# Performance work log

Hardware: AMD Instinct MI355X
Metric: run time of the kernel (lower is better)

The kernel has to match this reference:

```python
import jax, jax.numpy as jnp
import numpy as np

V, E, H = 32000, 512, 1024  # vocab, embed_dim, hidden_dim
N, T = 32, 256              # batch, seq_len


def setup_inputs() -> dict:
    key = jax.random.key(0)
    ks = jax.random.split(key, 8)
    s = 1.0 / np.sqrt(H)
    return {
        "words": jax.random.randint(ks[0], (N, T), 0, V),
        "hidden_state": jnp.zeros((N, H), jnp.float32),
        "embed_w": jax.random.uniform(ks[1], (V, E), minval=-1.0, maxval=1.0) * 0.1,
        "w_ih": jax.random.uniform(ks[2], (3 * H, E), minval=-s, maxval=s),
        "w_hh": jax.random.uniform(ks[3], (3 * H, H), minval=-s, maxval=s),
        "b_ih": jax.random.uniform(ks[4], (3 * H,), minval=-s, maxval=s),
        "b_hh": jax.random.uniform(ks[5], (3 * H,), minval=-s, maxval=s),
        "emit_w": jax.random.uniform(ks[6], (V, H), minval=-s, maxval=s),
        "emit_b": jnp.zeros((V,), jnp.float32),
    }


def reference(words, hidden_state, embed_w, w_ih, w_hh, b_ih, b_hh, emit_w, emit_b):
    n = words.shape[0]
    emb = embed_w[words]                      # [N, T, E]
    xs = (jnp.swapaxes(emb[:, :-1], 0, 1),    # [T-1, N, E] inputs x_{t-1}
          jnp.swapaxes(words[:, 1:], 0, 1))   # [T-1, N]    targets w_t

    def gru_cell(x, h):
        gi = x @ w_ih.T + b_ih                # [N, 3H]
        gh = h @ w_hh.T + b_hh                # [N, 3H]
        i_r, i_z, i_n = jnp.split(gi, 3, axis=-1)
        h_r, h_z, h_n = jnp.split(gh, 3, axis=-1)
        r = jax.nn.sigmoid(i_r + h_r)
        z = jax.nn.sigmoid(i_z + h_z)
        nn_ = jnp.tanh(i_n + r * h_n)
        return (1.0 - z) * nn_ + z * h

    def step(carry, inp):
        h, acc = carry
        x, w = inp
        h = gru_cell(x, h)
        logits = h @ emit_w.T + emit_b        # [N, V]
        logp = jax.nn.log_softmax(logits, axis=-1)
        ll = jnp.take_along_axis(logp, w[:, None], axis=1)[:, 0]  # [N]
        return (h, acc + ll), None

    acc0 = jnp.zeros((n,), hidden_state.dtype)
    (h_final, word_marginals), _ = jax.lax.scan(step, (hidden_state, acc0), xs)
    return word_marginals, h_final
```

## Files before the change

kernel.cpp:

```cpp
#include <hip/hip_runtime.h>
#include <cstdint>

#define V_    32000
#define E_    512
#define H_    1024
#define N_    32
#define T_    256
#define TS    255
#define NWG_B 64
#define CB_   250
#define RB_   64
#define MROW  8192
#define GI_CB 24

typedef _Float16 f16;
typedef _Float16 half8 __attribute__((ext_vector_type(8)));
typedef float floatx4 __attribute__((ext_vector_type(4)));
typedef unsigned long long u64;


__global__ void prep_emit16(const float* __restrict__ emit_w, f16* __restrict__ out) {
  const int64_t nchunk = (int64_t)V_ * H_ / 8;
  int64_t i = (int64_t)blockIdx.x * blockDim.x + threadIdx.x;
  for (; i < nchunk; i += (int64_t)gridDim.x * blockDim.x) {
    const float4* src = (const float4*)(emit_w + i * 8);
    float4 a = src[0], b = src[1];
    half8 h;
    h[0] = (f16)a.x; h[1] = (f16)a.y; h[2] = (f16)a.z; h[3] = (f16)a.w;
    h[4] = (f16)b.x; h[5] = (f16)b.y; h[6] = (f16)b.z; h[7] = (f16)b.w;
    *(half8*)(out + i * 8) = h;
  }
}

__global__ void prep_whh(const float* __restrict__ w_hh, f16* __restrict__ whh) {
  int idx = blockIdx.x * blockDim.x + threadIdx.x;
  if (idx >= 192 * 32 * 64) return;
  int lane = idx & 63;
  int kt   = (idx >> 6) & 31;
  int jt   = (idx >> 6) >> 5;
  int col  = jt * 16 + (lane & 15);
  int k0   = kt * 32 + (lane >> 4) * 8;
  const float* src = w_hh + (int64_t)col * H_ + k0;
  half8 h;
#pragma unroll
  for (int i = 0; i < 8; ++i) h[i] = (f16)src[i];
  *(half8*)(whh + (int64_t)idx * 8) = h;
}

__global__ void prep_wih16(const float* __restrict__ w_ih, f16* __restrict__ out) {
  int idx = blockIdx.x * blockDim.x + threadIdx.x;
  if (idx >= 3072 * 512 / 8) return;
  const float4* src = (const float4*)(w_ih + (int64_t)idx * 8);
  float4 a = src[0], b = src[1];
  half8 h;
  h[0] = (f16)a.x; h[1] = (f16)a.y; h[2] = (f16)a.z; h[3] = (f16)a.w;
  h[4] = (f16)b.x; h[5] = (f16)b.y; h[6] = (f16)b.z; h[7] = (f16)b.w;
  *(half8*)(out + (int64_t)idx * 8) = h;
}

__global__ void prep_xemb(const int* __restrict__ words, const float* __restrict__ embed_w,
                          f16* __restrict__ xemb) {
  int idx = blockIdx.x * blockDim.x + threadIdx.x;
  if (idx >= TS * N_ * (E_ / 8)) return;
  int u = idx & 63;
  int n = (idx >> 6) & 31;
  int t = idx >> 11;
  int word = words[n * T_ + t];
  const float* src = embed_w + (int64_t)word * E_ + u * 8;
  half8 h;
#pragma unroll
  for (int i = 0; i < 8; ++i) h[i] = (f16)src[i];
  *(half8*)(xemb + (int64_t)(t * N_ + n) * E_ + u * 8) = h;
}

__global__ void prep_init(const float* __restrict__ h0, f16* __restrict__ xh,
                          unsigned* __restrict__ slots) {
  int idx = blockIdx.x * blockDim.x + threadIdx.x;
  if (idx < N_ * H_) {
    f16 v = (f16)h0[idx];
    xh[idx] = v;
    xh[N_ * H_ + idx] = v;
  }
  if (idx < 1024) slots[idx] = 0;
}


#define LDK 72

__launch_bounds__(256, 2)
__global__ void gi_gemm(const f16* __restrict__ xemb, const f16* __restrict__ wih16,
                        f16* __restrict__ gi2) {
  const int cb = blockIdx.x % GI_CB;
  const int rb = blockIdx.x / GI_CB;
  const int tid = threadIdx.x;
  const int w = tid >> 6, lane = tid & 63;
  const int wm = w & 1, wn = w >> 1;
  const int l15 = lane & 15, l4 = lane >> 4;

  __shared__ f16 lA[128 * LDK];
  __shared__ f16 lB[128 * LDK];

  floatx4 acc[4][4];
#pragma unroll
  for (int mt = 0; mt < 4; ++mt)
#pragma unroll
    for (int nt = 0; nt < 4; ++nt) { acc[mt][nt][0] = 0.f; acc[mt][nt][1] = 0.f; acc[mt][nt][2] = 0.f; acc[mt][nt][3] = 0.f; }

  const f16* gA = xemb + (int64_t)rb * 128 * E_;
  const f16* gB = wih16 + (int64_t)cb * 128 * E_;

  for (int kb = 0; kb < 8; ++kb) {
    __syncthreads();
#pragma unroll
    for (int i = 0; i < 4; ++i) {
      int idx = i * 256 + tid;
      int row = idx >> 3, u = idx & 7;
      int64_t goff = (int64_t)row * E_ + kb * 64 + u * 8;
      *(half8*)(lA + row * LDK + u * 8) = *(const half8*)(gA + goff);
      *(half8*)(lB + row * LDK + u * 8) = *(const half8*)(gB + goff);
    }
    __syncthreads();
#pragma unroll
    for (int ks = 0; ks < 2; ++ks) {
      half8 af[4], bf[4];
#pragma unroll
      for (int mt = 0; mt < 4; ++mt)
        af[mt] = *(const half8*)(lA + (wm * 64 + mt * 16 + l15) * LDK + ks * 32 + l4 * 8);
#pragma unroll
      for (int nt = 0; nt < 4; ++nt)
        bf[nt] = *(const half8*)(lB + (wn * 64 + nt * 16 + l15) * LDK + ks * 32 + l4 * 8);
#pragma unroll
      for (int mt = 0; mt < 4; ++mt)
#pragma unroll
        for (int nt = 0; nt < 4; ++nt)
          acc[mt][nt] = __builtin_amdgcn_mfma_f32_16x16x32_f16(af[mt], bf[nt], acc[mt][nt], 0, 0, 0);
    }
  }

#pragma unroll
  for (int mt = 0; mt < 4; ++mt) {
#pragma unroll
    for (int r = 0; r < 4; ++r) {
      int g = rb * 128 + wm * 64 + mt * 16 + l4 * 4 + r;
      if (g < TS * N_) {
        int tt = g >> 5, n = g & 31;
        f16* gb = gi2 + ((int64_t)tt * 3072 + cb * 128 + wn * 64) * 32 + n;
#pragma unroll
        for (int nt = 0; nt < 4; ++nt)
          gb[(nt * 16 + l15) * 32] = (f16)acc[mt][nt][r];
      }
    }
  }
}


__device__ inline u64 aload64(const void* p) {
  return __hip_atomic_load((const u64*)p, __ATOMIC_RELAXED, __HIP_MEMORY_SCOPE_AGENT);
}
__device__ inline unsigned aload32(const void* p) {
  return __hip_atomic_load((const unsigned*)p, __ATOMIC_RELAXED, __HIP_MEMORY_SCOPE_AGENT);
}

__device__ inline void gbar3(unsigned* slots, unsigned tval, int b) {
  __syncthreads();
  if (threadIdx.x == 0) {
    __builtin_amdgcn_s_waitcnt(0);
    __hip_atomic_store(slots + b * 16, tval, __ATOMIC_RELAXED, __HIP_MEMORY_SCOPE_AGENT);
  }
  if (threadIdx.x < 64) {
    unsigned* my = slots + threadIdx.x * 16;
    while (__hip_atomic_load(my, __ATOMIC_RELAXED, __HIP_MEMORY_SCOPE_AGENT) < tval)
      __builtin_amdgcn_s_sleep(1);
  }
  __syncthreads();
}

__launch_bounds__(512, 1)
__global__ void phaseB(const f16* __restrict__ whh, const f16* __restrict__ gi2,
                       f16* __restrict__ xh, const float* __restrict__ b_ih,
                       const float* __restrict__ b_hh, f16* __restrict__ hall,
                       float* __restrict__ out, unsigned* __restrict__ slots) {
  const int b = blockIdx.x;
  const int tid = threadIdx.x;
  const int w = tid >> 6;
  const int lane = tid & 63;
  const int l15 = lane & 15, l4 = lane >> 4;

  __shared__ float part[8][32][49];

  const int n_g = tid & 31;
  const int jl = tid >> 5;
  const int j = b * 16 + jl;
  const float biasr = b_ih[j] + b_hh[j];
  const float biasz = b_ih[H_ + j] + b_hh[H_ + j];
  const float bihn = b_ih[2 * H_ + j];
  const float bhhn = b_hh[2 * H_ + j];

  half8 wf[3][4];
#pragma unroll
  for (int g = 0; g < 3; ++g) {
    int jt = g * 64 + b;
#pragma unroll
    for (int k = 0; k < 4; ++k)
      wf[g][k] = *(const half8*)(whh + (((int64_t)jt * 32 + (w * 4 + k)) * 64 + lane) * 8);
  }

  for (int t = 0; t < TS; ++t) {
    const f16* xh_rd = xh + (t & 1) * (N_ * H_);
    f16* xh_wr = xh + ((t + 1) & 1) * (N_ * H_);

    const f16* gbase = gi2 + (int64_t)t * 3072 * 32 + n_g;
    float gvr = (float)gbase[(int64_t)j * 32];
    float gvz = (float)gbase[(int64_t)(H_ + j) * 32];
    float gvn = (float)gbase[(int64_t)(2 * H_ + j) * 32];
    unsigned hraw = aload32(xh_rd + n_g * H_ + (j & ~1));
    unsigned short hbits = (jl & 1) ? (unsigned short)(hraw >> 16) : (unsigned short)(hraw & 0xffffu);
    float hold = (float)__builtin_bit_cast(f16, hbits);

    floatx4 acc[3][2];
#pragma unroll
    for (int g = 0; g < 3; ++g)
#pragma unroll
      for (int m = 0; m < 2; ++m) { acc[g][m][0] = 0.f; acc[g][m][1] = 0.f; acc[g][m][2] = 0.f; acc[g][m][3] = 0.f; }

    half8 a0[4], a1[4];
#pragma unroll
    for (int k = 0; k < 4; ++k) {
      const f16* base = xh_rd + (w * 4 + k) * 32 + l4 * 8;
      union { half8 h; u64 u[2]; } x0, x1;
      const u64* p0 = (const u64*)(base + (int64_t)l15 * H_);
      const u64* p1 = (const u64*)(base + (int64_t)(l15 + 16) * H_);
      x0.u[0] = aload64(p0); x0.u[1] = aload64(p0 + 1);
      x1.u[0] = aload64(p1); x1.u[1] = aload64(p1 + 1);
      a0[k] = x0.h; a1[k] = x1.h;
    }
#pragma unroll
    for (int k = 0; k < 4; ++k) {
#pragma unroll
      for (int g = 0; g < 3; ++g) {
        acc[g][0] = __builtin_amdgcn_mfma_f32_16x16x32_f16(a0[k], wf[g][k], acc[g][0], 0, 0, 0);
        acc[g][1] = __builtin_amdgcn_mfma_f32_16x16x32_f16(a1[k], wf[g][k], acc[g][1], 0, 0, 0);
      }
    }

#pragma unroll
    for (int g = 0; g < 3; ++g)
#pragma unroll
      for (int m = 0; m < 2; ++m)
#pragma unroll
        for (int r = 0; r < 4; ++r)
          part[w][m * 16 + l4 * 4 + r][g * 16 + l15] = acc[g][m][r];
    __syncthreads();

    float gr = biasr + gvr, gz = biasz + gvz, gin = bihn + gvn, ghn = bhhn;
#pragma unroll
    for (int ww = 0; ww < 8; ++ww) {
      gr += part[ww][n_g][jl];
      gz += part[ww][n_g][16 + jl];
      ghn += part[ww][n_g][32 + jl];
    }
    float rg = 1.f / (1.f + __expf(-gr));
    float zg = 1.f / (1.f + __expf(-gz));
    float nn = tanhf(gin + rg * ghn);
    float hnew = (1.f - zg) * nn + zg * hold;

    unsigned short hb = __builtin_bit_cast(unsigned short, (f16)hnew);
    unsigned other = (unsigned)__shfl_xor((int)(unsigned)hb, 32, 64);
    if (!(jl & 1)) {
      unsigned packed = (unsigned)hb | (other << 16);
      __hip_atomic_store((unsigned*)(xh_wr + n_g * H_ + j), packed,
                         __ATOMIC_RELAXED, __HIP_MEMORY_SCOPE_AGENT);
      *(unsigned*)(hall + ((int64_t)t * N_ + n_g) * H_ + j) = packed;
    }
    if (t == TS - 1) out[32 + n_g * H_ + j] = hnew;

    if (t < TS - 1) gbar3(slots, (unsigned)(t + 1), b);
  }
}


__launch_bounds__(256, 2)
__global__ void phaseC(const f16* __restrict__ hall, const f16* __restrict__ emit16,
                       const float* __restrict__ emit_b, float* __restrict__ spart) {
  const int cb = blockIdx.x % CB_;
  const int rb = blockIdx.x / CB_;
  const int tid = threadIdx.x;
  const int w = tid >> 6, lane = tid & 63;
  const int wm = w & 1, wn = w >> 1;
  const int l15 = lane & 15, l4 = lane >> 4;

  __shared__ f16 lA[128 * LDK];
  __shared__ f16 lB[128 * LDK];
  __shared__ float rs[2][128];

  floatx4 acc[4][4];
#pragma unroll
  for (int mt = 0; mt < 4; ++mt)
#pragma unroll
    for (int nt = 0; nt < 4; ++nt) { acc[mt][nt][0] = 0.f; acc[mt][nt][1] = 0.f; acc[mt][nt][2] = 0.f; acc[mt][nt][3] = 0.f; }

  const f16* gA = hall + (int64_t)rb * 128 * H_;
  const f16* gB = emit16 + (int64_t)cb * 128 * H_;

  for (int kb = 0; kb < 16; ++kb) {
    __syncthreads();
#pragma unroll
    for (int i = 0; i < 4; ++i) {
      int idx = i * 256 + tid;
      int row = idx >> 3, u = idx & 7;
      int64_t goff = (int64_t)row * H_ + kb * 64 + u * 8;
      *(half8*)(lA + row * LDK + u * 8) = *(const half8*)(gA + goff);
      *(half8*)(lB + row * LDK + u * 8) = *(const half8*)(gB + goff);
    }
    __syncthreads();
#pragma unroll
    for (int ks = 0; ks < 2; ++ks) {
      half8 af[4], bf[4];
#pragma unroll
      for (int mt = 0; mt < 4; ++mt)
        af[mt] = *(const half8*)(lA + (wm * 64 + mt * 16 + l15) * LDK + ks * 32 + l4 * 8);
#pragma unroll
      for (int nt = 0; nt < 4; ++nt)
        bf[nt] = *(const half8*)(lB + (wn * 64 + nt * 16 + l15) * LDK + ks * 32 + l4 * 8);
#pragma unroll
      for (int mt = 0; mt < 4; ++mt)
#pragma unroll
        for (int nt = 0; nt < 4; ++nt)
          acc[mt][nt] = __builtin_amdgcn_mfma_f32_16x16x32_f16(af[mt], bf[nt], acc[mt][nt], 0, 0, 0);
    }
  }

  float eb[4];
#pragma unroll
  for (int nt = 0; nt < 4; ++nt) eb[nt] = emit_b[cb * 128 + wn * 64 + nt * 16 + l15];

#pragma unroll
  for (int mt = 0; mt < 4; ++mt) {
#pragma unroll
    for (int r = 0; r < 4; ++r) {
      float s = 0.f;
#pragma unroll
      for (int nt = 0; nt < 4; ++nt) s += __expf(acc[mt][nt][r] + eb[nt]);
#pragma unroll
      for (int off = 1; off < 16; off <<= 1) s += __shfl_xor(s, off, 64);
      if (l15 == 0) rs[wn][wm * 64 + mt * 16 + l4 * 4 + r] = s;
    }
  }
  __syncthreads();
  if (tid < 128)
    spart[(int64_t)cb * MROW + rb * 128 + tid] = rs[0][tid] + rs[1][tid];
}


__global__ void target_dots(const f16* __restrict__ hall, const f16* __restrict__ emit16,
                            const int* __restrict__ words, const float* __restrict__ emit_b,
                            float* __restrict__ tlog) {
  int r = blockIdx.x * 4 + (threadIdx.x >> 6);
  if (r >= TS * N_) return;
  int lane = threadIdx.x & 63;
  int t = r >> 5, n = r & 31;
  int tgt = words[n * T_ + t + 1];
  const f16* ha = hall + (int64_t)r * H_;
  const f16* ebp = emit16 + (int64_t)tgt * H_;
  float s = 0.f;
#pragma unroll
  for (int c = 0; c < 2; ++c) {
    int k = c * 512 + lane * 8;
    half8 a = *(const half8*)(ha + k);
    half8 b = *(const half8*)(ebp + k);
#pragma unroll
    for (int i = 0; i < 8; ++i) s += (float)a[i] * (float)b[i];
  }
#pragma unroll
  for (int off = 1; off < 64; off <<= 1) s += __shfl_xor(s, off, 64);
  if (lane == 0) tlog[r] = s + emit_b[tgt];
}

__global__ void reduce_lse(const float* __restrict__ spart, const float* __restrict__ tlog,
                           float* __restrict__ lval) {
  int r = blockIdx.x * blockDim.x + threadIdx.x;
  if (r >= TS * N_) return;
  float s = 0.f;
  for (int cb = 0; cb < CB_; ++cb) s += spart[(int64_t)cb * MROW + r];
  lval[r] = tlog[r] - logf(s);
}

__global__ void finalize(const float* __restrict__ lval, float* __restrict__ out) {
  __shared__ float ps[8][32];
  int n = threadIdx.x & 31, sl = threadIdx.x >> 5;
  float s = 0.f;
  for (int i = 0; i < 32; ++i) {
    int t = sl * 32 + i;
    if (t < TS) s += lval[t * N_ + n];
  }
  ps[sl][n] = s;
  __syncthreads();
  if (threadIdx.x < 32) {
    float tot = 0.f;
#pragma unroll
    for (int k = 0; k < 8; ++k) tot += ps[k][threadIdx.x];
    out[threadIdx.x] = tot;
  }
}


extern "C" void kernel_launch(void* const* d_in, const int* in_sizes, int n_in,
                              void* d_out, int out_size, void* d_ws, size_t ws_size,
                              hipStream_t stream) {
  (void)in_sizes; (void)n_in; (void)out_size; (void)ws_size;
  const int*   words   = (const int*)d_in[0];
  const float* h0      = (const float*)d_in[1];
  const float* embed_w = (const float*)d_in[2];
  const float* w_ih    = (const float*)d_in[3];
  const float* w_hh    = (const float*)d_in[4];
  const float* b_ih    = (const float*)d_in[5];
  const float* b_hh    = (const float*)d_in[6];
  const float* emit_w  = (const float*)d_in[7];
  const float* emit_b  = (const float*)d_in[8];
  float* out = (float*)d_out;

  char* ws = (char*)d_ws;
  f16*      big    = (f16*)(ws + 0);
  f16*      gi2    = big;
  f16*      emit16 = big;
  f16*      whh    = (f16*)(ws + 65536000);
  f16*      wih16  = (f16*)(ws + 71827456);
  float*    spart  = (float*)(ws + 71827456);
  f16*      xemb   = (f16*)(ws + 74973184);
  f16*      xh     = (f16*)(ws + 83361792);
  f16*      hall   = (f16*)(ws + 83492864);
  float*    tlog   = (float*)(ws + 100270080);
  float*    lval   = (float*)(ws + 100302720);
  unsigned* slots  = (unsigned*)(ws + 100335360);

  hipLaunchKernelGGL(prep_whh, dim3(1536), dim3(256), 0, stream, w_hh, whh);
  hipLaunchKernelGGL(prep_wih16, dim3(768), dim3(256), 0, stream, w_ih, wih16);
  hipLaunchKernelGGL(prep_xemb, dim3(2040), dim3(256), 0, stream, words, embed_w, xemb);
  hipLaunchKernelGGL(prep_init, dim3(128), dim3(256), 0, stream, h0, xh, slots);
  hipLaunchKernelGGL(gi_gemm, dim3(RB_ * GI_CB), dim3(256), 0, stream, xemb, wih16, gi2);
  hipLaunchKernelGGL(phaseB, dim3(NWG_B), dim3(512), 0, stream, whh, gi2, xh, b_ih, b_hh, hall, out, slots);
  hipLaunchKernelGGL(prep_emit16, dim3(4096), dim3(256), 0, stream, emit_w, emit16);
  hipLaunchKernelGGL(phaseC, dim3(RB_ * CB_), dim3(256), 0, stream, hall, emit16, emit_b, spart);
  hipLaunchKernelGGL(target_dots, dim3((TS * N_ + 3) / 4), dim3(256), 0, stream, hall, emit16, words, emit_b, tlog);
  hipLaunchKernelGGL(reduce_lse, dim3((TS * N_ + 255) / 256), dim3(256), 0, stream, spart, tlog, lval);
  hipLaunchKernelGGL(finalize, dim3(1), dim3(256), 0, stream, lval, out);
}
```

Measured before the change: 2.728 ms.

## Replace grid barrier with per-element step-tagged hidden state flags

Drops the per-timestep global barrier in the persistent GRU recurrence kernel. Each fp16 hidden value is now stored next to a 16-bit step tag inside 64-bit words. Consumers spin until all the words they read carry the expected tag, so each block waits only on the data it needs instead of on every block. This removes the barrier's atomic round trips but doubles the size of the hidden-state exchange buffer and adds polling and unpacking work. It also reuses the xemb workspace region for the tagged buffer, which is safe only because the launch order was changed so gi_gemm runs first.

After: 4.452 ms. 1.63x slower.

```diff
diff --git a/kernel.cpp b/kernel.cpp
--- a/kernel.cpp
+++ b/kernel.cpp
@@ -73,15 +73,16 @@
   *(half8*)(xemb + (int64_t)(t * N_ + n) * E_ + u * 8) = h;
 }
 
-__global__ void prep_init(const float* __restrict__ h0, f16* __restrict__ xh,
-                          unsigned* __restrict__ slots) {
+__global__ void prep_init(const float* __restrict__ h0, u64* __restrict__ xt) {
   int idx = blockIdx.x * blockDim.x + threadIdx.x;
-  if (idx < N_ * H_) {
-    f16 v = (f16)h0[idx];
-    xh[idx] = v;
-    xh[N_ * H_ + idx] = v;
-  }
-  if (idx < 1024) slots[idx] = 0;
+  if (idx < N_ * H_ / 2) {
+    int n = idx >> 9;
+    int p = idx & 511;
+    unsigned short e = __builtin_bit_cast(unsigned short, (f16)h0[n * H_ + 2 * p]);
+    unsigned short o = __builtin_bit_cast(unsigned short, (f16)h0[n * H_ + 2 * p + 1]);
+    xt[idx] = (u64)(unsigned)e | ((u64)(unsigned)o << 32);
+    xt[N_ * H_ / 2 + idx] = 0;
+  }
 }
 
 
@@ -157,36 +158,19 @@
 __device__ inline u64 aload64(const void* p) {
   return __hip_atomic_load((const u64*)p, __ATOMIC_RELAXED, __HIP_MEMORY_SCOPE_AGENT);
 }
-__device__ inline unsigned aload32(const void* p) {
-  return __hip_atomic_load((const unsigned*)p, __ATOMIC_RELAXED, __HIP_MEMORY_SCOPE_AGENT);
-}
-
-__device__ inline void gbar3(unsigned* slots, unsigned tval, int b) {
-  __syncthreads();
-  if (threadIdx.x == 0) {
-    __builtin_amdgcn_s_waitcnt(0);
-    __hip_atomic_store(slots + b * 16, tval, __ATOMIC_RELAXED, __HIP_MEMORY_SCOPE_AGENT);
-  }
-  if (threadIdx.x < 64) {
-    unsigned* my = slots + threadIdx.x * 16;
-    while (__hip_atomic_load(my, __ATOMIC_RELAXED, __HIP_MEMORY_SCOPE_AGENT) < tval)
-      __builtin_amdgcn_s_sleep(1);
-  }
-  __syncthreads();
-}
 
 __launch_bounds__(512, 1)
 __global__ void phaseB(const f16* __restrict__ whh, const f16* __restrict__ gi2,
-                       f16* __restrict__ xh, const float* __restrict__ b_ih,
+                       u64* __restrict__ xt, const float* __restrict__ b_ih,
                        const float* __restrict__ b_hh, f16* __restrict__ hall,
-                       float* __restrict__ out, unsigned* __restrict__ slots) {
+                       float* __restrict__ out) {
   const int b = blockIdx.x;
   const int tid = threadIdx.x;
   const int w = tid >> 6;
   const int lane = tid & 63;
   const int l15 = lane & 15, l4 = lane >> 4;
 
-  __shared__ float part[8][32][49];
+  __shared__ float part[2][8][32][49];
 
   const int n_g = tid & 31;
   const int jl = tid >> 5;
@@ -205,17 +189,72 @@
       wf[g][k] = *(const half8*)(whh + (((int64_t)jt * 32 + (w * 4 + k)) * 64 + lane) * 8);
   }
 
+  {
+  }
+  u64 w0 = xt[n_g * (H_ / 2) + (j >> 1)];
+  unsigned lohi0 = (jl & 1) ? (unsigned)(w0 >> 32) : (unsigned)w0;
+  float hold = (float)__builtin_bit_cast(f16, (unsigned short)(lohi0 & 0xffffu));
+
   for (int t = 0; t < TS; ++t) {
-    const f16* xh_rd = xh + (t & 1) * (N_ * H_);
-    f16* xh_wr = xh + ((t + 1) & 1) * (N_ * H_);
+    const u64* xr = xt + (t & 1) * (N_ * (H_ / 2));
+    u64* xw = xt + ((t + 1) & 1) * (N_ * (H_ / 2));
+    const unsigned tg = (unsigned)t;
 
     const f16* gbase = gi2 + (int64_t)t * 3072 * 32 + n_g;
     float gvr = (float)gbase[(int64_t)j * 32];
     float gvz = (float)gbase[(int64_t)(H_ + j) * 32];
     float gvn = (float)gbase[(int64_t)(2 * H_ + j) * 32];
-    unsigned hraw = aload32(xh_rd + n_g * H_ + (j & ~1));
-    unsigned short hbits = (jl & 1) ? (unsigned short)(hraw >> 16) : (unsigned short)(hraw & 0xffffu);
-    float hold = (float)__builtin_bit_cast(f16, hbits);
+
+    half8 a0[4], a1[4];
+    {
+      u64 v[4][2][4];
+      bool ok[4][2] = {{false, false}, {false, false}, {false, false}, {false, false}};
+      int nleft = 8;
+      const u64* rp0 = xr + (int64_t)l15 * (H_ / 2) + l4 * 4;
+      const u64* rp1 = xr + (int64_t)(l15 + 16) * (H_ / 2) + l4 * 4;
+      while (true) {
+#pragma unroll
+        for (int k = 0; k < 4; ++k) {
+          if (!ok[k][0]) {
+            const u64* p = rp0 + (w * 4 + k) * 16;
+#pragma unroll
+            for (int q = 0; q < 4; ++q) v[k][0][q] = aload64(p + q);
+          }
+          if (!ok[k][1]) {
+            const u64* p = rp1 + (w * 4 + k) * 16;
+#pragma unroll
+            for (int q = 0; q < 4; ++q) v[k][1][q] = aload64(p + q);
+          }
+        }
+#pragma unroll
+        for (int k = 0; k < 4; ++k)
+#pragma unroll
+          for (int r = 0; r < 2; ++r) {
+            if (!ok[k][r]) {
+              bool f = true;
+#pragma unroll
+              for (int q = 0; q < 4; ++q) {
+                u64 x = v[k][r][q];
+                f = f && (((unsigned)(x >> 16) & 0xffffu) == tg) && ((unsigned)(x >> 48) == tg);
+              }
+              if (f) { ok[k][r] = true; --nleft; }
+            }
+          }
+        if (nleft == 0) break;
+        __builtin_amdgcn_s_sleep(1);
+      }
+#pragma unroll
+      for (int k = 0; k < 4; ++k) {
+        union { half8 h; unsigned u[4]; } t0, t1;
+#pragma unroll
+        for (int q = 0; q < 4; ++q) {
+          u64 x0 = v[k][0][q], x1 = v[k][1][q];
+          t0.u[q] = ((unsigned)x0 & 0xffffu) | (((unsigned)(x0 >> 32)) << 16);
+          t1.u[q] = ((unsigned)x1 & 0xffffu) | (((unsigned)(x1 >> 32)) << 16);
+        }
+        a0[k] = t0.h; a1[k] = t1.h;
+      }
+    }
 
     floatx4 acc[3][2];
 #pragma unroll
@@ -223,17 +262,6 @@
 #pragma unroll
       for (int m = 0; m < 2; ++m) { acc[g][m][0] = 0.f; acc[g][m][1] = 0.f; acc[g][m][2] = 0.f; acc[g][m][3] = 0.f; }
 
-    half8 a0[4], a1[4];
-#pragma unroll
-    for (int k = 0; k < 4; ++k) {
-      const f16* base = xh_rd + (w * 4 + k) * 32 + l4 * 8;
-      union { half8 h; u64 u[2]; } x0, x1;
-      const u64* p0 = (const u64*)(base + (int64_t)l15 * H_);
-      const u64* p1 = (const u64*)(base + (int64_t)(l15 + 16) * H_);
-      x0.u[0] = aload64(p0); x0.u[1] = aload64(p0 + 1);
-      x1.u[0] = aload64(p1); x1.u[1] = aload64(p1 + 1);
-      a0[k] = x0.h; a1[k] = x1.h;
-    }
 #pragma unroll
     for (int k = 0; k < 4; ++k) {
 #pragma unroll
@@ -243,21 +271,22 @@
       }
     }
 
+    float (*pp)[32][49] = part[t & 1];
 #pragma unroll
     for (int g = 0; g < 3; ++g)
 #pragma unroll
       for (int m = 0; m < 2; ++m)
 #pragma unroll
         for (int r = 0; r < 4; ++r)
-          part[w][m * 16 + l4 * 4 + r][g * 16 + l15] = acc[g][m][r];
+          pp[w][m * 16 + l4 * 4 + r][g * 16 + l15] = acc[g][m][r];
     __syncthreads();
 
     float gr = biasr + gvr, gz = biasz + gvz, gin = bihn + gvn, ghn = bhhn;
 #pragma unroll
     for (int ww = 0; ww < 8; ++ww) {
-      gr += part[ww][n_g][jl];
-      gz += part[ww][n_g][16 + jl];
-      ghn += part[ww][n_g][32 + jl];
+      gr += pp[ww][n_g][jl];
+      gz += pp[ww][n_g][16 + jl];
+      ghn += pp[ww][n_g][32 + jl];
     }
     float rg = 1.f / (1.f + __expf(-gr));
     float zg = 1.f / (1.f + __expf(-gz));
@@ -265,16 +294,18 @@
     float hnew = (1.f - zg) * nn + zg * hold;
 
     unsigned short hb = __builtin_bit_cast(unsigned short, (f16)hnew);
-    unsigned other = (unsigned)__shfl_xor((int)(unsigned)hb, 32, 64);
+    unsigned other = (unsigned)__shfl_xor((int)(unsigned)hb, 32, 64) & 0xffffu;
     if (!(jl & 1)) {
-      unsigned packed = (unsigned)hb | (other << 16);
-      __hip_atomic_store((unsigned*)(xh_wr + n_g * H_ + j), packed,
+      unsigned lo = ((tg + 1) << 16) | (unsigned)hb;
+      unsigned hi = ((tg + 1) << 16) | other;
+      u64 word = (u64)lo | ((u64)hi << 32);
+      __hip_atomic_store(xw + n_g * (H_ / 2) + (j >> 1), word,
                          __ATOMIC_RELAXED, __HIP_MEMORY_SCOPE_AGENT);
-      *(unsigned*)(hall + ((int64_t)t * N_ + n_g) * H_ + j) = packed;
+      *(unsigned*)(hall + ((int64_t)t * N_ + n_g) * H_ + j) = (unsigned)hb | (other << 16);
     }
     if (t == TS - 1) out[32 + n_g * H_ + j] = hnew;
 
-    if (t < TS - 1) gbar3(slots, (unsigned)(t + 1), b);
+    hold = (float)(f16)hnew;
   }
 }
 
@@ -427,18 +458,17 @@
   f16*      wih16  = (f16*)(ws + 71827456);
   float*    spart  = (float*)(ws + 71827456);
   f16*      xemb   = (f16*)(ws + 74973184);
-  f16*      xh     = (f16*)(ws + 83361792);
+  u64*      xt     = (u64*)(ws + 74973184);
   f16*      hall   = (f16*)(ws + 83492864);
   float*    tlog   = (float*)(ws + 100270080);
   float*    lval   = (float*)(ws + 100302720);
-  unsigned* slots  = (unsigned*)(ws + 100335360);
 
   hipLaunchKernelGGL(prep_whh, dim3(1536), dim3(256), 0, stream, w_hh, whh);
   hipLaunchKernelGGL(prep_wih16, dim3(768), dim3(256), 0, stream, w_ih, wih16);
   hipLaunchKernelGGL(prep_xemb, dim3(2040), dim3(256), 0, stream, words, embed_w, xemb);
-  hipLaunchKernelGGL(prep_init, dim3(128), dim3(256), 0, stream, h0, xh, slots);
   hipLaunchKernelGGL(gi_gemm, dim3(RB_ * GI_CB), dim3(256), 0, stream, xemb, wih16, gi2);
-  hipLaunchKernelGGL(phaseB, dim3(NWG_B), dim3(512), 0, stream, whh, gi2, xh, b_ih, b_hh, hall, out, slots);
+  hipLaunchKernelGGL(prep_init, dim3(64), dim3(256), 0, stream, h0, xt);
+  hipLaunchKernelGGL(phaseB, dim3(NWG_B), dim3(512), 0, stream, whh, gi2, xt, b_ih, b_hh, hall, out);
   hipLaunchKernelGGL(prep_emit16, dim3(4096), dim3(256), 0, stream, emit_w, emit16);
   hipLaunchKernelGGL(phaseC, dim3(RB_ * CB_), dim3(256), 0, stream, hall, emit16, emit_b, spart);
   hipLaunchKernelGGL(target_dots, dim3((TS * N_ + 3) / 4), dim3(256), 0, stream, hall, emit16, words, emit_b, tlog);
```

## Use direct global-to-LDS loads with XOR swizzle and remap phaseC workgroups

Applied to the files above, without the earlier changes.

The emission GEMM's tile loads now go straight from global memory into LDS through global_load_lds with 16-byte transfers, skipping the register round trip. The padded LDS stride is replaced by an XOR-swizzled 64-wide layout, which keeps MFMA fragment reads free of bank conflicts. Workgroup IDs are also remapped so that groups sharing the same emit-weight column block are spread across the XCDs. The intended gains are fewer VGPRs and instructions per load and better L2 reuse. The risk is that the load path remains synchronous and unpipelined, so any benefit depends on how much load issue overhead was actually limiting.

Result: faster. 2.594 ms (-4.9%).

```diff
diff --git a/kernel.cpp b/kernel.cpp
--- a/kernel.cpp
+++ b/kernel.cpp
@@ -279,18 +279,24 @@
 }
 
 
+__device__ inline void gload_lds16(const f16* g, f16* l) {
+  __builtin_amdgcn_global_load_lds((const __attribute__((address_space(1))) void*)g,
+                                   (__attribute__((address_space(3))) void*)l, 16, 0, 0);
+}
+
 __launch_bounds__(256, 2)
 __global__ void phaseC(const f16* __restrict__ hall, const f16* __restrict__ emit16,
                        const float* __restrict__ emit_b, float* __restrict__ spart) {
-  const int cb = blockIdx.x % CB_;
-  const int rb = blockIdx.x / CB_;
+  const int wgid = (blockIdx.x & 7) * 2000 + (blockIdx.x >> 3);
+  const int cb = wgid >> 6;
+  const int rb = wgid & 63;
   const int tid = threadIdx.x;
   const int w = tid >> 6, lane = tid & 63;
   const int wm = w & 1, wn = w >> 1;
   const int l15 = lane & 15, l4 = lane >> 4;
 
-  __shared__ f16 lA[128 * LDK];
-  __shared__ f16 lB[128 * LDK];
+  __shared__ f16 lA[128 * 64];
+  __shared__ f16 lB[128 * 64];
   __shared__ float rs[2][128];
 
   floatx4 acc[4][4];
@@ -302,26 +308,30 @@
   const f16* gA = hall + (int64_t)rb * 128 * H_;
   const f16* gB = emit16 + (int64_t)cb * 128 * H_;
 
+  const int lrow8 = lane >> 3;
+  const int sc = (lane & 7) ^ lrow8;
+  const int rdx = (l15 & 7) << 3;
+
   for (int kb = 0; kb < 16; ++kb) {
     __syncthreads();
 #pragma unroll
     for (int i = 0; i < 4; ++i) {
-      int idx = i * 256 + tid;
-      int row = idx >> 3, u = idx & 7;
-      int64_t goff = (int64_t)row * H_ + kb * 64 + u * 8;
-      *(half8*)(lA + row * LDK + u * 8) = *(const half8*)(gA + goff);
-      *(half8*)(lB + row * LDK + u * 8) = *(const half8*)(gB + goff);
+      const int r0 = w * 32 + i * 8;
+      const int64_t goff = (int64_t)(r0 + lrow8) * H_ + kb * 64 + sc * 8;
+      gload_lds16(gA + goff, lA + r0 * 64);
+      gload_lds16(gB + goff, lB + r0 * 64);
     }
     __syncthreads();
 #pragma unroll
     for (int ks = 0; ks < 2; ++ks) {
       half8 af[4], bf[4];
+      const int col = (ks * 32 + l4 * 8) ^ rdx;
 #pragma unroll
       for (int mt = 0; mt < 4; ++mt)
-        af[mt] = *(const half8*)(lA + (wm * 64 + mt * 16 + l15) * LDK + ks * 32 + l4 * 8);
+        af[mt] = *(const half8*)(lA + (wm * 64 + mt * 16 + l15) * 64 + col);
 #pragma unroll
       for (int nt = 0; nt < 4; ++nt)
-        bf[nt] = *(const half8*)(lB + (wn * 64 + nt * 16 + l15) * LDK + ks * 32 + l4 * 8);
+        bf[nt] = *(const half8*)(lB + (wn * 64 + nt * 16 + l15) * 64 + col);
 #pragma unroll
       for (int mt = 0; mt < 4; ++mt)
 #pragma unroll
```
